# Performance work log

Hardware: AMD Instinct MI355X
Metric: run time of the kernel (lower is better)

Reference implementation:

```python
import jax, jax.numpy as jnp
import numpy as np

N_NODES = 50000
N_EDGES = 800000
IN_FEATS = 128
OUT_FEATS = 128


def setup_inputs() -> dict:
    key = jax.random.key(0)
    k_feat, k_src, k_dst, k_w1, k_w2, k_lw = jax.random.split(key, 6)
    feat = jax.random.normal(k_feat, (N_NODES, IN_FEATS), dtype=jnp.float32)
    src_idx = jax.random.randint(k_src, (N_EDGES,), 0, N_NODES, dtype=jnp.int64 if jax.config.jax_enable_x64 else jnp.int32)
    dst_idx = jax.random.randint(k_dst, (N_EDGES,), 0, N_NODES, dtype=jnp.int64 if jax.config.jax_enable_x64 else jnp.int32)
    # xavier-uniform-ish scales
    w1_lim = float(np.sqrt(6.0 / (2 * IN_FEATS + IN_FEATS)))
    w2_lim = float(np.sqrt(6.0 / (IN_FEATS + OUT_FEATS)))
    lw_lim = float(np.sqrt(2.0) * np.sqrt(6.0 / (IN_FEATS + OUT_FEATS)))
    weight1 = jax.random.uniform(k_w1, (2 * IN_FEATS, IN_FEATS), jnp.float32, -w1_lim, w1_lim)
    weight2 = jax.random.uniform(k_w2, (IN_FEATS, OUT_FEATS), jnp.float32, -w2_lim, w2_lim)
    loop_weight = jax.random.uniform(k_lw, (IN_FEATS, OUT_FEATS), jnp.float32, -lw_lim, lw_lim)
    bias = jnp.zeros((OUT_FEATS,), dtype=jnp.float32)
    return {
        "feat": feat,
        "src_idx": src_idx,
        "dst_idx": dst_idx,
        "weight1": weight1,
        "weight2": weight2,
        "loop_weight": loop_weight,
        "bias": bias,
    }


def reference(feat, src_idx, dst_idx, weight1, weight2, loop_weight, bias):
    # Gather per-edge src/dst features and concat: [E, 2*d]
    feat_msg = jnp.concatenate([feat[src_idx], feat[dst_idx]], axis=-1)
    # 2-layer edge MLP: relu(msg @ W1) @ W2 -> [E, out]
    e_msg = jnp.matmul(jax.nn.relu(jnp.matmul(feat_msg, weight1)), weight2)
    # Scatter-sum to destination nodes: [N, out]
    rst = jax.ops.segment_sum(e_msg, dst_idx, num_segments=feat.shape[0])
    # bias + residual loop message
    rst = rst + bias + jnp.matmul(feat, loop_weight)
    return rst
```

## Files before the change

kernel.cpp:

```cpp
#include <hip/hip_runtime.h>

typedef __attribute__((ext_vector_type(8))) unsigned short ushort8v;
typedef __attribute__((ext_vector_type(8))) short short8v;
typedef __attribute__((ext_vector_type(4))) float f32x4;

#define CAP 64
#define BINSTRIDE 2560

__device__ inline unsigned short f2bf(float f) {
    union { float f; unsigned u; } v; v.f = f;
    unsigned u = v.u;
    unsigned r = (u + 0x7FFFu + ((u >> 16) & 1u)) >> 16;
    return (unsigned short)r;
}
__device__ inline float bf2f(unsigned short h) {
    union { unsigned u; float f; } v; v.u = ((unsigned)h) << 16;
    return v.f;
}
__device__ inline unsigned pkbf(float lo, float hi) {
    unsigned r;
    asm("v_cvt_pk_bf16_f32 %0, %1, %2" : "=v"(r) : "v"(lo), "v"(hi));
    return r;
}

__global__ __launch_bounds__(256) void prep_weights(
    const float* __restrict__ W1, const float* __restrict__ W2,
    const float* __restrict__ LW,
    unsigned short* __restrict__ W1t, unsigned short* __restrict__ W3t,
    int* __restrict__ binCur, int NBINS) {
    int tid = threadIdx.x;
    if (blockIdx.x == 0)
        for (int j = tid; j < NBINS; j += 256) binCur[j] = 0;
    int i = blockIdx.x * 256 + tid;
    if (i < 32768) {
        int jj = i >> 7, k = i & 127;
        float v = (jj < 128) ? W1[k * 128 + jj] : W1[(128 + k) * 128 + (jj - 128)];
        W1t[i] = f2bf(v);
    } else {
        int i2 = i - 32768;
        int n = i2 >> 8, k = i2 & 255;
        float v = (k < 128) ? W2[k * 128 + n] : LW[(k - 128) * 128 + n];
        W3t[i2] = f2bf(v);
    }
}

__global__ __launch_bounds__(256) void gemm1_bin(
    const float* __restrict__ feat, const unsigned short* __restrict__ W1t,
    unsigned short* __restrict__ AB,
    const int* __restrict__ src, const int* __restrict__ dst,
    int* __restrict__ binCur, unsigned* __restrict__ binPairs,
    int E, int NC, int NT2, int M, int NBINS) {
    __shared__ unsigned short smem[2 * 128 * 64];
    const int tid = threadIdx.x;
    const int bid = blockIdx.x;
    const int r5 = bid % 5;

    if (r5 < 4) {
        int g = (bid / 5) * 4 + r5;
        if (g >= NT2) return;
        int m0 = (g >> 1) * 128, n0 = (g & 1) * 128;
        const int lane = tid & 63, w = tid >> 6;
        const int wr = w >> 1, wc = w & 1;
        const int q = lane >> 4, ln = lane & 15;
        unsigned short* As = smem;
        unsigned short* Bs = smem + 128 * 64;

        f32x4 acc[4][4];
#pragma unroll
        for (int i = 0; i < 4; i++)
#pragma unroll
            for (int j = 0; j < 4; j++) acc[i][j] = (f32x4)0.f;

        for (int kk = 0; kk < 128; kk += 64) {
#pragma unroll
            for (int i = 0; i < 4; i++) {
                int id = i * 256 + tid;
                int r = id >> 3, bb = id & 7, gr = m0 + r;
                unsigned short* dstp = As + r * 64 + ((bb ^ (r & 7)) * 8);
                float4 lo = make_float4(0.f, 0.f, 0.f, 0.f), hi = lo;
                if (gr < M) {
                    const float* p = feat + (size_t)gr * 128 + kk + bb * 8;
                    lo = *(const float4*)p;
                    hi = *(const float4*)(p + 4);
                }
                *(uint4*)dstp = make_uint4(pkbf(lo.x, lo.y), pkbf(lo.z, lo.w),
                                           pkbf(hi.x, hi.y), pkbf(hi.z, hi.w));
            }
#pragma unroll
            for (int i = 0; i < 4; i++) {
                int id = i * 256 + tid;
                int r = id >> 3, bb = id & 7;
                ushort8v v = *(const ushort8v*)(W1t + (size_t)(n0 + r) * 128 + kk + bb * 8);
                *(ushort8v*)(Bs + r * 64 + ((bb ^ (r & 7)) * 8)) = v;
            }
            __syncthreads();
#pragma unroll
            for (int ks = 0; ks < 2; ks++) {
                short8v af[4], bv[4];
#pragma unroll
                for (int ti = 0; ti < 4; ti++) {
                    int m = wr * 64 + ti * 16 + ln;
                    int blk = (ks * 4 + q) ^ (m & 7);
                    af[ti] = *(const short8v*)(As + m * 64 + blk * 8);
                }
#pragma unroll
                for (int tj = 0; tj < 4; tj++) {
                    int n = wc * 64 + tj * 16 + ln;
                    int blk = (ks * 4 + q) ^ (n & 7);
                    bv[tj] = *(const short8v*)(Bs + n * 64 + blk * 8);
                }
#pragma unroll
                for (int ti = 0; ti < 4; ti++)
#pragma unroll
                    for (int tj = 0; tj < 4; tj++)
                        acc[ti][tj] = __builtin_amdgcn_mfma_f32_16x16x32_bf16(
                            af[ti], bv[tj], acc[ti][tj], 0, 0, 0);
            }
            if (kk == 0) __syncthreads();
        }
#pragma unroll
        for (int ti = 0; ti < 4; ti++) {
            int rowb = m0 + wr * 64 + ti * 16 + q * 4;
#pragma unroll
            for (int tj = 0; tj < 4; tj++) {
                int col = n0 + wc * 64 + tj * 16 + ln;
                f32x4 c = acc[ti][tj];
#pragma unroll
                for (int r = 0; r < 4; r++) {
                    int row = rowb + r;
                    if (row < M)
                        AB[(size_t)row * 256 + col] = f2bf(c[r]);
                }
            }
        }
    } else {
        int chunk = bid / 5;
        if (chunk >= NC) return;
        int* hist = (int*)smem;
        int* bse = hist + 512;
        for (int j = tid; j < NBINS; j += 256) hist[j] = 0;

        int s[16], d[16];
        int base = chunk * 4096;
#pragma unroll
        for (int i = 0; i < 4; i++) {
            int e = base + i * 1024 + tid * 4;
            if (e + 3 < E) {
                int4 dv = *(const int4*)(dst + e);
                int4 sv = *(const int4*)(src + e);
                d[i * 4 + 0] = dv.x; d[i * 4 + 1] = dv.y;
                d[i * 4 + 2] = dv.z; d[i * 4 + 3] = dv.w;
                s[i * 4 + 0] = sv.x; s[i * 4 + 1] = sv.y;
                s[i * 4 + 2] = sv.z; s[i * 4 + 3] = sv.w;
            } else {
#pragma unroll
                for (int k = 0; k < 4; k++) {
                    int ee = e + k;
                    if (ee < E) { d[i * 4 + k] = dst[ee]; s[i * 4 + k] = src[ee]; }
                    else d[i * 4 + k] = -1;
                }
            }
        }
        __syncthreads();
#pragma unroll
        for (int k = 0; k < 16; k++)
            if (d[k] >= 0) atomicAdd(&hist[d[k] >> 7], 1);
        __syncthreads();
        for (int j = tid; j < NBINS; j += 256) {
            int c = hist[j];
            bse[j] = c ? atomicAdd(&binCur[j], c) : 0;
            hist[j] = 0;
        }
        __syncthreads();
#pragma unroll
        for (int k = 0; k < 16; k++) {
            if (d[k] < 0) continue;
            int b = d[k] >> 7;
            int p = bse[b] + atomicAdd(&hist[b], 1);
            if (p < BINSTRIDE)
                binPairs[(size_t)b * BINSTRIDE + p] =
                    ((unsigned)(d[k] & 127) << 16) | (unsigned)s[k];
        }
    }
}

__global__ __launch_bounds__(256) void build_buckets(
    const int* __restrict__ binCur, const unsigned* __restrict__ binPairs,
    int* __restrict__ cur, unsigned short* __restrict__ eSrc,
    int N, int NBINS) {
    __shared__ unsigned pairs[BINSTRIDE];
    __shared__ int deg[128], rnk[128];
    int b = blockIdx.x, tid = threadIdx.x;
    if (b >= NBINS) return;
    int cnt = min(binCur[b], BINSTRIDE);
    if (tid < 128) { deg[tid] = 0; rnk[tid] = 0; }
    __syncthreads();
    for (int i = tid; i < cnt; i += 256) {
        unsigned pr = binPairs[(size_t)b * BINSTRIDE + i];
        pairs[i] = pr;
        atomicAdd(&deg[pr >> 16], 1);
    }
    __syncthreads();
    int node0 = b << 7;
    if (tid < 128 && node0 + tid < N) cur[node0 + tid] = deg[tid];
    for (int i = tid; i < cnt; i += 256) {
        unsigned pr = pairs[i];
        int dl = pr >> 16;
        int pos = atomicAdd(&rnk[dl], 1);
        if (pos < CAP)
            eSrc[(size_t)(node0 + dl) * CAP + pos] = (unsigned short)(pr & 0xFFFF);
    }
}

__global__ __launch_bounds__(256) void gather_kernel(
    const unsigned short* __restrict__ AB, const int* __restrict__ cur,
    const unsigned short* __restrict__ eSrc,
    unsigned short* __restrict__ S2, int N) {
    int wid = (blockIdx.x * 256 + threadIdx.x) >> 6;
    int lane = threadIdx.x & 63;
    if (wid >= N) return;
    int num = min(cur[wid], CAP);
    size_t start = (size_t)wid * CAP;
    int qw = lane >> 4, lq = lane & 15;

    ushort8v b8 = *(const ushort8v*)(AB + (size_t)wid * 256 + 128 + lq * 8);
    float b[8], p[8];
#pragma unroll
    for (int e = 0; e < 8; e++) { b[e] = bf2f(b8[e]); p[e] = 0.f; }

    int mySrc = (lane < num) ? (int)eSrc[start + lane] : 0;

    for (int j = 0; j < num; j += 16) {
        ushort8v v[4];
        float msk[4];
#pragma unroll
        for (int u = 0; u < 4; u++) {
            int idx = j + 4 * u + qw;
            int s = __shfl(mySrc, idx);
            bool ok = idx < num;
            msk[u] = ok ? 1.f : 0.f;
            int saddr = ok ? s : 0;
            v[u] = *(const ushort8v*)(AB + (size_t)saddr * 256 + lq * 8);
        }
#pragma unroll
        for (int u = 0; u < 4; u++)
#pragma unroll
            for (int e = 0; e < 8; e++)
                p[e] += msk[u] * fmaxf(bf2f(v[u][e]) + b[e], 0.f);
    }
#pragma unroll
    for (int e = 0; e < 8; e++) {
        p[e] += __shfl_xor(p[e], 16);
        p[e] += __shfl_xor(p[e], 32);
    }
    if (qw == 0) {
        ushort8v o;
#pragma unroll
        for (int e = 0; e < 8; e += 2) {
            unsigned pk = pkbf(p[e], p[e + 1]);
            o[e] = (unsigned short)(pk & 0xFFFF);
            o[e + 1] = (unsigned short)(pk >> 16);
        }
        *(ushort8v*)(S2 + (size_t)wid * 128 + lq * 8) = o;
    }
}

__global__ __launch_bounds__(256) void gemm2_kernel(
    const unsigned short* __restrict__ S2, const float* __restrict__ feat,
    const unsigned short* __restrict__ W3t,
    float* __restrict__ out, const float* __restrict__ bias, int M) {
    __shared__ unsigned short smem[2 * 128 * 64];
    unsigned short* As = smem;
    unsigned short* Bs = smem + 128 * 64;
    const int tid = threadIdx.x;
    const int lane = tid & 63, w = tid >> 6;
    const int wr = w >> 1, wc = w & 1;
    const int q = lane >> 4, ln = lane & 15;
    const int m0 = blockIdx.x * 128;

    f32x4 acc[4][4];
#pragma unroll
    for (int i = 0; i < 4; i++)
#pragma unroll
        for (int j = 0; j < 4; j++) acc[i][j] = (f32x4)0.f;

    for (int kk = 0; kk < 256; kk += 64) {
        const bool aF32 = (kk >= 128);
#pragma unroll
        for (int i = 0; i < 4; i++) {
            int id = i * 256 + tid;
            int r = id >> 3, bb = id & 7, gr = m0 + r;
            unsigned short* dstp = As + r * 64 + ((bb ^ (r & 7)) * 8);
            if (aF32) {
                float4 lo = make_float4(0.f, 0.f, 0.f, 0.f), hi = lo;
                if (gr < M) {
                    const float* p = feat + (size_t)gr * 128 + (kk - 128) + bb * 8;
                    lo = *(const float4*)p;
                    hi = *(const float4*)(p + 4);
                }
                *(uint4*)dstp = make_uint4(pkbf(lo.x, lo.y), pkbf(lo.z, lo.w),
                                           pkbf(hi.x, hi.y), pkbf(hi.z, hi.w));
            } else {
                ushort8v v = (ushort8v)(unsigned short)0;
                if (gr < M) v = *(const ushort8v*)(S2 + (size_t)gr * 128 + kk + bb * 8);
                *(ushort8v*)dstp = v;
            }
        }
#pragma unroll
        for (int i = 0; i < 4; i++) {
            int id = i * 256 + tid;
            int r = id >> 3, bb = id & 7;
            ushort8v v = *(const ushort8v*)(W3t + (size_t)r * 256 + kk + bb * 8);
            *(ushort8v*)(Bs + r * 64 + ((bb ^ (r & 7)) * 8)) = v;
        }
        __syncthreads();
#pragma unroll
        for (int ks = 0; ks < 2; ks++) {
            short8v af[4], bv[4];
#pragma unroll
            for (int ti = 0; ti < 4; ti++) {
                int m = wr * 64 + ti * 16 + ln;
                int blk = (ks * 4 + q) ^ (m & 7);
                af[ti] = *(const short8v*)(As + m * 64 + blk * 8);
            }
#pragma unroll
            for (int tj = 0; tj < 4; tj++) {
                int n = wc * 64 + tj * 16 + ln;
                int blk = (ks * 4 + q) ^ (n & 7);
                bv[tj] = *(const short8v*)(Bs + n * 64 + blk * 8);
            }
#pragma unroll
            for (int ti = 0; ti < 4; ti++)
#pragma unroll
                for (int tj = 0; tj < 4; tj++)
                    acc[ti][tj] = __builtin_amdgcn_mfma_f32_16x16x32_bf16(
                        af[ti], bv[tj], acc[ti][tj], 0, 0, 0);
        }
        if (kk + 64 < 256) __syncthreads();
    }

#pragma unroll
    for (int ti = 0; ti < 4; ti++) {
        int rowb = m0 + wr * 64 + ti * 16 + q * 4;
#pragma unroll
        for (int tj = 0; tj < 4; tj++) {
            int col = wc * 64 + tj * 16 + ln;
            f32x4 c = acc[ti][tj];
            float bv = bias[col];
#pragma unroll
            for (int r = 0; r < 4; r++) {
                int row = rowb + r;
                if (row < M)
                    out[(size_t)row * 128 + col] = c[r] + bv;
            }
        }
    }
}

extern "C" void kernel_launch(void* const* d_in, const int* in_sizes, int n_in,
                              void* d_out, int out_size, void* d_ws, size_t ws_size,
                              hipStream_t stream) {
    const float* feat = (const float*)d_in[0];
    const int* src = (const int*)d_in[1];
    const int* dst = (const int*)d_in[2];
    const float* W1 = (const float*)d_in[3];
    const float* W2 = (const float*)d_in[4];
    const float* LW = (const float*)d_in[5];
    const float* bias = (const float*)d_in[6];
    float* out = (float*)d_out;

    const int N = in_sizes[0] / 128;
    const int E = in_sizes[1];
    const int NBINS = (N + 127) / 128;

    char* ws = (char*)d_ws;
    unsigned short* S2 = (unsigned short*)ws;
    size_t off = (size_t)N * 128 * 2;
    unsigned short* AB = (unsigned short*)(ws + off);
    off += (size_t)N * 256 * 2;
    unsigned short* W1t = (unsigned short*)(ws + off);
    off += (size_t)256 * 128 * 2;
    unsigned short* W3t = (unsigned short*)(ws + off);
    off += (size_t)128 * 256 * 2;
    int* cur = (int*)(ws + off);
    off += (size_t)N * 4;
    unsigned short* eSrc = (unsigned short*)(ws + off);
    off += (size_t)N * CAP * 2;
    int* binCur = (int*)(ws + off);
    off += (size_t)NBINS * 4;
    unsigned* binPairs = (unsigned*)(ws + off);
    off += (size_t)NBINS * BINSTRIDE * 4;

    prep_weights<<<256, 256, 0, stream>>>(W1, W2, LW, W1t, W3t, binCur, NBINS);

    int NT2 = ((N + 127) / 128) * 2;
    int NC = (E + 4095) / 4096;
    int NG = (NT2 + 3) / 4;
    int mx = NG > NC ? NG : NC;
    gemm1_bin<<<5 * mx, 256, 0, stream>>>(
        feat, W1t, AB, src, dst, binCur, binPairs, E, NC, NT2, N, NBINS);

    build_buckets<<<NBINS, 256, 0, stream>>>(binCur, binPairs, cur, eSrc, N, NBINS);

    gather_kernel<<<(N + 3) / 4, 256, 0, stream>>>(AB, cur, eSrc, S2, N);

    gemm2_kernel<<<(N + 127) / 128, 256, 0, stream>>>(S2, feat, W3t, out, bias, N);
}
```

Before: 159.7 us.

## Retile both GEMMs to 64-row tiles, gemm1 covering full 256 output columns

gemm1 now gives each block a 64x256 output tile instead of a 128x128 tile. Each feature row is then read and converted to bf16 once rather than twice, at the cost of loading the whole W1t into shared memory per block. gemm2 switches from 128x128 to 64x128 tiles, doubling the block count (about 782 vs 391) so the work spreads across more CUs, with half the accumulators per wave. Shared memory per block grows in gemm1 and the B-tile staging work per output row increases.

```diff
diff --git a/kernel.cpp b/kernel.cpp
--- a/kernel.cpp
+++ b/kernel.cpp
@@ -49,21 +49,20 @@
     unsigned short* __restrict__ AB,
     const int* __restrict__ src, const int* __restrict__ dst,
     int* __restrict__ binCur, unsigned* __restrict__ binPairs,
-    int E, int NC, int NT2, int M, int NBINS) {
-    __shared__ unsigned short smem[2 * 128 * 64];
+    int E, int NC, int NT, int M, int NBINS) {
+    __shared__ unsigned short smem[(64 + 256) * 64];
     const int tid = threadIdx.x;
     const int bid = blockIdx.x;
     const int r5 = bid % 5;
 
     if (r5 < 4) {
         int g = (bid / 5) * 4 + r5;
-        if (g >= NT2) return;
-        int m0 = (g >> 1) * 128, n0 = (g & 1) * 128;
+        if (g >= NT) return;
+        int m0 = g * 64;
         const int lane = tid & 63, w = tid >> 6;
-        const int wr = w >> 1, wc = w & 1;
         const int q = lane >> 4, ln = lane & 15;
         unsigned short* As = smem;
-        unsigned short* Bs = smem + 128 * 64;
+        unsigned short* Bs = smem + 64 * 64;
 
         f32x4 acc[4][4];
 #pragma unroll
@@ -73,7 +72,7 @@
 
         for (int kk = 0; kk < 128; kk += 64) {
 #pragma unroll
-            for (int i = 0; i < 4; i++) {
+            for (int i = 0; i < 2; i++) {
                 int id = i * 256 + tid;
                 int r = id >> 3, bb = id & 7, gr = m0 + r;
                 unsigned short* dstp = As + r * 64 + ((bb ^ (r & 7)) * 8);
@@ -87,10 +86,10 @@
                                            pkbf(hi.x, hi.y), pkbf(hi.z, hi.w));
             }
 #pragma unroll
-            for (int i = 0; i < 4; i++) {
+            for (int i = 0; i < 8; i++) {
                 int id = i * 256 + tid;
                 int r = id >> 3, bb = id & 7;
-                ushort8v v = *(const ushort8v*)(W1t + (size_t)(n0 + r) * 128 + kk + bb * 8);
+                ushort8v v = *(const ushort8v*)(W1t + (size_t)r * 128 + kk + bb * 8);
                 *(ushort8v*)(Bs + r * 64 + ((bb ^ (r & 7)) * 8)) = v;
             }
             __syncthreads();
@@ -99,13 +98,13 @@
                 short8v af[4], bv[4];
 #pragma unroll
                 for (int ti = 0; ti < 4; ti++) {
-                    int m = wr * 64 + ti * 16 + ln;
+                    int m = ti * 16 + ln;
                     int blk = (ks * 4 + q) ^ (m & 7);
                     af[ti] = *(const short8v*)(As + m * 64 + blk * 8);
                 }
 #pragma unroll
                 for (int tj = 0; tj < 4; tj++) {
-                    int n = wc * 64 + tj * 16 + ln;
+                    int n = w * 64 + tj * 16 + ln;
                     int blk = (ks * 4 + q) ^ (n & 7);
                     bv[tj] = *(const short8v*)(Bs + n * 64 + blk * 8);
                 }
@@ -120,10 +119,10 @@
         }
 #pragma unroll
         for (int ti = 0; ti < 4; ti++) {
-            int rowb = m0 + wr * 64 + ti * 16 + q * 4;
+            int rowb = m0 + ti * 16 + q * 4;
 #pragma unroll
             for (int tj = 0; tj < 4; tj++) {
-                int col = n0 + wc * 64 + tj * 16 + ln;
+                int col = w * 64 + tj * 16 + ln;
                 f32x4 c = acc[ti][tj];
 #pragma unroll
                 for (int r = 0; r < 4; r++) {
@@ -269,25 +268,24 @@
     const unsigned short* __restrict__ S2, const float* __restrict__ feat,
     const unsigned short* __restrict__ W3t,
     float* __restrict__ out, const float* __restrict__ bias, int M) {
-    __shared__ unsigned short smem[2 * 128 * 64];
+    __shared__ unsigned short smem[(64 + 128) * 64];
     unsigned short* As = smem;
-    unsigned short* Bs = smem + 128 * 64;
+    unsigned short* Bs = smem + 64 * 64;
     const int tid = threadIdx.x;
     const int lane = tid & 63, w = tid >> 6;
-    const int wr = w >> 1, wc = w & 1;
     const int q = lane >> 4, ln = lane & 15;
-    const int m0 = blockIdx.x * 128;
-
-    f32x4 acc[4][4];
+    const int m0 = blockIdx.x * 64;
+
+    f32x4 acc[4][2];
 #pragma unroll
     for (int i = 0; i < 4; i++)
 #pragma unroll
-        for (int j = 0; j < 4; j++) acc[i][j] = (f32x4)0.f;
+        for (int j = 0; j < 2; j++) acc[i][j] = (f32x4)0.f;
 
     for (int kk = 0; kk < 256; kk += 64) {
         const bool aF32 = (kk >= 128);
 #pragma unroll
-        for (int i = 0; i < 4; i++) {
+        for (int i = 0; i < 2; i++) {
             int id = i * 256 + tid;
             int r = id >> 3, bb = id & 7, gr = m0 + r;
             unsigned short* dstp = As + r * 64 + ((bb ^ (r & 7)) * 8);
@@ -316,23 +314,23 @@
         __syncthreads();
 #pragma unroll
         for (int ks = 0; ks < 2; ks++) {
-            short8v af[4], bv[4];
+            short8v af[4], bv[2];
 #pragma unroll
             for (int ti = 0; ti < 4; ti++) {
-                int m = wr * 64 + ti * 16 + ln;
+                int m = ti * 16 + ln;
                 int blk = (ks * 4 + q) ^ (m & 7);
                 af[ti] = *(const short8v*)(As + m * 64 + blk * 8);
             }
 #pragma unroll
-            for (int tj = 0; tj < 4; tj++) {
-                int n = wc * 64 + tj * 16 + ln;
+            for (int tj = 0; tj < 2; tj++) {
+                int n = w * 32 + tj * 16 + ln;
                 int blk = (ks * 4 + q) ^ (n & 7);
                 bv[tj] = *(const short8v*)(Bs + n * 64 + blk * 8);
             }
 #pragma unroll
             for (int ti = 0; ti < 4; ti++)
 #pragma unroll
-                for (int tj = 0; tj < 4; tj++)
+                for (int tj = 0; tj < 2; tj++)
                     acc[ti][tj] = __builtin_amdgcn_mfma_f32_16x16x32_bf16(
                         af[ti], bv[tj], acc[ti][tj], 0, 0, 0);
         }
@@ -341,10 +339,10 @@
 
 #pragma unroll
     for (int ti = 0; ti < 4; ti++) {
-        int rowb = m0 + wr * 64 + ti * 16 + q * 4;
-#pragma unroll
-        for (int tj = 0; tj < 4; tj++) {
-            int col = wc * 64 + tj * 16 + ln;
+        int rowb = m0 + ti * 16 + q * 4;
+#pragma unroll
+        for (int tj = 0; tj < 2; tj++) {
+            int col = w * 32 + tj * 16 + ln;
             f32x4 c = acc[ti][tj];
             float bv = bias[col];
 #pragma unroll
@@ -393,16 +391,16 @@
 
     prep_weights<<<256, 256, 0, stream>>>(W1, W2, LW, W1t, W3t, binCur, NBINS);
 
-    int NT2 = ((N + 127) / 128) * 2;
+    int NT = (N + 63) / 64;
     int NC = (E + 4095) / 4096;
-    int NG = (NT2 + 3) / 4;
+    int NG = (NT + 3) / 4;
     int mx = NG > NC ? NG : NC;
     gemm1_bin<<<5 * mx, 256, 0, stream>>>(
-        feat, W1t, AB, src, dst, binCur, binPairs, E, NC, NT2, N, NBINS);
+        feat, W1t, AB, src, dst, binCur, binPairs, E, NC, NT, N, NBINS);
 
     build_buckets<<<NBINS, 256, 0, stream>>>(binCur, binPairs, cur, eSrc, N, NBINS);
 
     gather_kernel<<<(N + 3) / 4, 256, 0, stream>>>(AB, cur, eSrc, S2, N);
 
-    gemm2_kernel<<<(N + 127) / 128, 256, 0, stream>>>(S2, feat, W3t, out, bias, N);
-}
+    gemm2_kernel<<<(N + 63) / 64, 256, 0, stream>>>(S2, feat, W3t, out, bias, N);
+}
```

After: 155.4 us. 1.03x faster.
